# Optimization experiments

Hardware: AMD Instinct MI355X
Metric: run time of the kernel (lower is better)

The kernel has to match this reference:

```python
import jax, jax.numpy as jnp
import numpy as np

H = 3584          # hidden_size
NH = 28           # num query heads
NKV = 4           # num kv heads
HD = H // NH      # head_dim = 128
I = 18944         # intermediate_size
EPS = 1e-6
THETA = 1000000.0


def setup_inputs() -> dict:
    key = jax.random.key(0)
    ks = jax.random.split(key, 16)
    B, S = 1, 2048
    s = 0.02
    inp = {
        "hidden_states": jax.random.normal(ks[0], (B, S, H), jnp.float32),
        "position_ids": jnp.broadcast_to(jnp.arange(S, dtype=jnp.int32)[None, :], (B, S)),
        "q_w": jax.random.normal(ks[1], (NH * HD, H), jnp.float32) * s,
        "q_b": jax.random.normal(ks[2], (NH * HD,), jnp.float32) * s,
        "k_w": jax.random.normal(ks[3], (NKV * HD, H), jnp.float32) * s,
        "k_b": jax.random.normal(ks[4], (NKV * HD,), jnp.float32) * s,
        "v_w": jax.random.normal(ks[5], (NKV * HD, H), jnp.float32) * s,
        "v_b": jax.random.normal(ks[6], (NKV * HD,), jnp.float32) * s,
        "o_w": jax.random.normal(ks[7], (H, NH * HD), jnp.float32) * s,
        "gate_w": jax.random.normal(ks[8], (I, H), jnp.float32) * s,
        "up_w": jax.random.normal(ks[9], (I, H), jnp.float32) * s,
        "down_w": jax.random.normal(ks[10], (H, I), jnp.float32) * s,
        "ln1_w": jnp.ones((H,), jnp.float32),
        "ln2_w": jnp.ones((H,), jnp.float32),
    }
    return inp


def _rms_norm(x, w):
    var = jnp.mean(jnp.square(x), axis=-1, keepdims=True)
    return x * jax.lax.rsqrt(var + EPS) * w


def _rope_cos_sin(position_ids):
    # inv_freq: [HD/2]
    inv_freq = 1.0 / (THETA ** (jnp.arange(0, HD, 2, dtype=jnp.float32) / HD))
    ang = position_ids.astype(jnp.float32)[..., None] * inv_freq  # [B,S,HD/2]
    emb = jnp.concatenate([ang, ang], axis=-1)                     # [B,S,HD]
    return jnp.cos(emb)[:, None], jnp.sin(emb)[:, None]            # [B,1,S,HD]


def _rotate_half(x):
    x1, x2 = x[..., : HD // 2], x[..., HD // 2 :]
    return jnp.concatenate([-x2, x1], axis=-1)


def _forward(hidden_states, position_ids, q_w, q_b, k_w, k_b, v_w, v_b,
             o_w, gate_w, up_w, down_w, ln1_w, ln2_w):
    B, S, _ = hidden_states.shape
    residual = hidden_states
    x = _rms_norm(hidden_states, ln1_w)

    q = jnp.einsum("bsh,dh->bsd", x, q_w) + q_b   # [B,S,NH*HD]
    k = jnp.einsum("bsh,dh->bsd", x, k_w) + k_b   # [B,S,NKV*HD]
    v = jnp.einsum("bsh,dh->bsd", x, v_w) + v_b

    q = q.reshape(B, S, NH, HD).transpose(0, 2, 1, 3)    # [B,NH,S,HD]
    k = k.reshape(B, S, NKV, HD).transpose(0, 2, 1, 3)   # [B,NKV,S,HD]
    v = v.reshape(B, S, NKV, HD).transpose(0, 2, 1, 3)

    cos, sin = _rope_cos_sin(position_ids)
    q = q * cos + _rotate_half(q) * sin
    k = k * cos + _rotate_half(k) * sin

    # GQA: group query heads per kv head (NH = NKV * G)
    G = NH // NKV
    qg = q.reshape(B, NKV, G, S, HD)
    scores = jnp.einsum("bhgsd,bhtd->bhgst", qg, k) / jnp.sqrt(jnp.float32(HD))
    probs = jax.nn.softmax(scores, axis=-1)               # no causal mask in source
    attn = jnp.einsum("bhgst,bhtd->bhgsd", probs, v)      # [B,NKV,G,S,HD]
    attn = attn.reshape(B, NH, S, HD).transpose(0, 2, 1, 3).reshape(B, S, H)

    attn_out = jnp.einsum("bsd,hd->bsh", attn, o_w)
    hidden = residual + attn_out

    residual = hidden
    x = _rms_norm(hidden, ln2_w)
    gate = jax.nn.silu(jnp.einsum("bsh,ih->bsi", x, gate_w))
    up = jnp.einsum("bsh,ih->bsi", x, up_w)
    mlp = jnp.einsum("bsi,hi->bsh", gate * up, down_w)
    return residual + mlp


def reference(hidden_states, position_ids, q_w, q_b, k_w, k_b, v_w, v_b,
              o_w, gate_w, up_w, down_w, ln1_w, ln2_w):
    return _forward(hidden_states, position_ids, q_w, q_b, k_w, k_b, v_w, v_b,
                    o_w, gate_w, up_w, down_w, ln1_w, ln2_w)
```

## Files before the change

### kernel.cpp

```cpp
#include <hip/hip_runtime.h>
#include <hip/hip_bf16.h>
#include <stdint.h>

#define S_LEN 2048
#define HDIM  3584
#define NHEAD 28
#define NKVH  4
#define HDHD  128
#define IDIM  18944

typedef __attribute__((ext_vector_type(8))) short short8;
typedef __attribute__((ext_vector_type(4))) float floatx4;
typedef __attribute__((ext_vector_type(4))) unsigned int uint4v;

__device__ __forceinline__ unsigned short f2bf(float f) {
  union { float f; unsigned int u; } v; v.f = f;
  unsigned int r = v.u + 0x7fffu + ((v.u >> 16) & 1u);
  return (unsigned short)(r >> 16);
}
__device__ __forceinline__ float bf2f(unsigned short h) {
  union { unsigned int u; float f; } v; v.u = ((unsigned int)h) << 16;
  return v.f;
}
__device__ __forceinline__ unsigned int pk2(float a, float b) {
  __hip_bfloat162 h = __float22bfloat162_rn(make_float2(a, b));
  union { __hip_bfloat162 h; unsigned int u; } c; c.h = h; return c.u;
}

__device__ __forceinline__ void gload_lds16(const void* g, void* l) {
  __builtin_amdgcn_global_load_lds(
      (const __attribute__((address_space(1))) void*)g,
      (__attribute__((address_space(3))) void*)l, 16, 0, 0);
}

__device__ __forceinline__ int xcd_remap(int id, int total) {
  return (id & 7) * (total >> 3) + (id >> 3);
}

__device__ __forceinline__ void store_out(int MODE, void* outp, const void* aux,
                                          size_t oidx, float v) {
  if (MODE == 0) {
    ((float*)outp)[oidx] = v;
  } else if (MODE == 1) {
    ((unsigned short*)outp)[oidx] = f2bf(v);
  } else if (MODE == 2) {
    ((float*)outp)[oidx] = v + ((const float*)aux)[oidx];
  } else {
    float gt = bf2f(((const unsigned short*)aux)[oidx]);
    float sg = gt / (1.f + __expf(-gt));
    ((unsigned short*)outp)[oidx] = f2bf(sg * v);
  }
}

template<int MODE, bool BIAS>
__global__ __launch_bounds__(256)
void gemm_bf(const unsigned short* __restrict__ A, int lda,
             const unsigned short* __restrict__ W,
             const float* __restrict__ bias,
             void* __restrict__ outp, int ldo, int col0,
             const void* __restrict__ aux, int K)
{
  const int g  = xcd_remap(blockIdx.x, gridDim.x);
  const int mb = g & 15;
  const int nb = g >> 4;
  const int t = threadIdx.x;
  const int w = t >> 6, l = t & 63, lg = l >> 4, lc = l & 15;
  const int wr = w >> 1, wc = w & 1;

  __shared__ __align__(16) unsigned short As[128 * 64];
  __shared__ __align__(16) unsigned short Ws[128 * 64];

  floatx4 acc[4][4] = {};

  const char* Ablk = (const char*)(A + (size_t)mb * 128 * lda);
  const char* Wblk = (const char*)(W + (size_t)nb * 128 * K);

  const int s_row = t >> 3;
  const int s_scb = (((t & 7) ^ ((t >> 3) & 7)) << 4);
  const int r_sw  = (lc & 7) << 4;

  const size_t abytes = (size_t)lda * 2;
  const size_t wbytes = (size_t)K * 2;
  const int nk = K >> 6;
  for (int kt = 0; kt < nk; ++kt) {
    #pragma unroll
    for (int i = 0; i < 4; ++i)
      gload_lds16(Ablk + (size_t)(i * 32 + s_row) * abytes + (size_t)kt * 128 + s_scb,
                  (char*)As + i * 4096 + t * 16);
    #pragma unroll
    for (int i = 0; i < 4; ++i)
      gload_lds16(Wblk + (size_t)(i * 32 + s_row) * wbytes + (size_t)kt * 128 + s_scb,
                  (char*)Ws + i * 4096 + t * 16);
    __syncthreads();
    #pragma unroll
    for (int kk = 0; kk < 2; ++kk) {
      short8 afr[4], bfr[4];
      #pragma unroll
      for (int m = 0; m < 4; ++m)
        afr[m] = *(const short8*)((const char*)As + (wr*64 + m*16 + lc) * 128
                                 + ((kk*64 + lg*16) ^ r_sw));
      #pragma unroll
      for (int n = 0; n < 4; ++n)
        bfr[n] = *(const short8*)((const char*)Ws + (wc*64 + n*16 + lc) * 128
                                  + ((kk*64 + lg*16) ^ r_sw));
      #pragma unroll
      for (int m = 0; m < 4; ++m)
        #pragma unroll
        for (int n = 0; n < 4; ++n)
          acc[m][n] = __builtin_amdgcn_mfma_f32_16x16x32_bf16(afr[m], bfr[n], acc[m][n], 0, 0, 0);
    }
    __syncthreads();
  }

  float bv[4] = {0.f, 0.f, 0.f, 0.f};
  if (BIAS) {
    #pragma unroll
    for (int n = 0; n < 4; ++n) bv[n] = bias[nb*128 + wc*64 + n*16 + lc];
  }
  #pragma unroll
  for (int m = 0; m < 4; ++m) {
    #pragma unroll
    for (int n = 0; n < 4; ++n) {
      const int colg = col0 + nb*128 + wc*64 + n*16 + lc;
      #pragma unroll
      for (int j = 0; j < 4; ++j) {
        const int rowg = mb*128 + wr*64 + m*16 + lg*4 + j;
        store_out(MODE, outp, aux, (size_t)rowg * ldo + colg, acc[m][n][j] + bv[n]);
      }
    }
  }
}

template<int MODE, bool BIAS>
__global__ __launch_bounds__(256, 2)
void gemm_w(const unsigned short* __restrict__ A, int lda,
            const unsigned short* __restrict__ W,
            const float* __restrict__ bias,
            void* __restrict__ outp, int ldo, int col0,
            const void* __restrict__ aux, int K)
{
  const int g  = xcd_remap(blockIdx.x, gridDim.x);
  const int mb = g & 7;
  const int nb = g >> 3;
  const int t  = threadIdx.x;
  const int w  = t >> 6, l = t & 63, lg = l >> 4, lc = l & 15;
  const int wr = w >> 1, wc = w & 1;

  __shared__ __align__(16) unsigned short As[256 * 64];
  __shared__ __align__(16) unsigned short Bs[128 * 64];

  floatx4 acc[8][4] = {};

  const char* Ablk = (const char*)(A + (size_t)mb * 256 * lda);
  const char* Wblk = (const char*)(W + (size_t)nb * 128 * K);

  const int s_row = t >> 3;
  const int s_scb = (((t & 7) ^ ((t >> 3) & 7)) << 4);
  const int r_sw  = (lc & 7) << 4;

  const size_t abytes = (size_t)lda * 2;
  const size_t wbytes = (size_t)K * 2;
  const int nk = K >> 6;

  for (int kt = 0; kt < nk; ++kt) {
    const char* asrc = Ablk + (size_t)kt * 128 + s_scb;
    #pragma unroll
    for (int i = 0; i < 8; ++i)
      gload_lds16(asrc + (size_t)(i * 32 + s_row) * abytes,
                  (char*)As + i * 4096 + t * 16);
    const char* wsrc = Wblk + (size_t)kt * 128 + s_scb;
    #pragma unroll
    for (int i = 0; i < 4; ++i)
      gload_lds16(wsrc + (size_t)(i * 32 + s_row) * wbytes,
                  (char*)Bs + i * 4096 + t * 16);
    __syncthreads();
    #pragma unroll
    for (int kk = 0; kk < 2; ++kk) {
      const int ko = (kk * 64 + lg * 16) ^ r_sw;
      short8 bfr[4];
      #pragma unroll
      for (int n = 0; n < 4; ++n)
        bfr[n] = *(const short8*)((const char*)Bs + (wc*64 + n*16 + lc) * 128 + ko);
      #pragma unroll
      for (int m = 0; m < 8; ++m) {
        short8 af = *(const short8*)((const char*)As + (wr*128 + m*16 + lc) * 128 + ko);
        #pragma unroll
        for (int n = 0; n < 4; ++n)
          acc[m][n] = __builtin_amdgcn_mfma_f32_16x16x32_bf16(af, bfr[n], acc[m][n], 0, 0, 0);
      }
    }
    __syncthreads();
  }

  float bv[4] = {0.f, 0.f, 0.f, 0.f};
  if (BIAS) {
    #pragma unroll
    for (int n = 0; n < 4; ++n) bv[n] = bias[nb*128 + wc*64 + n*16 + lc];
  }
  #pragma unroll
  for (int m = 0; m < 8; ++m) {
    #pragma unroll
    for (int n = 0; n < 4; ++n) {
      const int colg = col0 + nb*128 + wc*64 + n*16 + lc;
      #pragma unroll
      for (int j = 0; j < 4; ++j) {
        const int rowg = mb*256 + wr*128 + m*16 + lg*4 + j;
        store_out(MODE, outp, aux, (size_t)rowg * ldo + colg, acc[m][n][j] + bv[n]);
      }
    }
  }
}

__global__ __launch_bounds__(256)
void cvt_bf16_kernel(const float* __restrict__ in, unsigned short* __restrict__ out, int n8)
{
  int i = blockIdx.x * 256 + threadIdx.x;
  const int stride = gridDim.x * 256;
  for (; i < n8; i += stride) {
    floatx4 a = *(const floatx4*)(in + (size_t)i * 8);
    floatx4 b = *(const floatx4*)(in + (size_t)i * 8 + 4);
    uint4v p;
    p[0] = pk2(a[0], a[1]); p[1] = pk2(a[2], a[3]);
    p[2] = pk2(b[0], b[1]); p[3] = pk2(b[2], b[3]);
    *(uint4v*)(out + (size_t)i * 8) = p;
  }
}

__global__ void pack_bias_kernel(const float* __restrict__ qb, const float* __restrict__ kb,
                                 const float* __restrict__ vb, float* __restrict__ o)
{
  int i = blockIdx.x * 256 + threadIdx.x;
  if (i < 3584) o[i] = qb[i];
  else if (i < 4096) o[i] = kb[i - 3584];
  else if (i < 4608) o[i] = vb[i - 4096];
}

__global__ __launch_bounds__(448)
void rmsnorm_kernel(const float* __restrict__ x, const float* __restrict__ wgt,
                    unsigned short* __restrict__ out)
{
  const int row = blockIdx.x, t = threadIdx.x;
  const float* xp = x + (size_t)row * HDIM + t * 8;
  floatx4 a = *(const floatx4*)xp;
  floatx4 b = *(const floatx4*)(xp + 4);
  float ss = a[0]*a[0]+a[1]*a[1]+a[2]*a[2]+a[3]*a[3]
           + b[0]*b[0]+b[1]*b[1]+b[2]*b[2]+b[3]*b[3];
  #pragma unroll
  for (int mk = 1; mk < 64; mk <<= 1) ss += __shfl_xor(ss, mk, 64);
  __shared__ float wsum[8];
  if ((t & 63) == 0) wsum[t >> 6] = ss;
  __syncthreads();
  float tot = 0.f;
  #pragma unroll
  for (int i = 0; i < 7; ++i) tot += wsum[i];
  const float sc = rsqrtf(tot * (1.f / 3584.f) + 1e-6f);
  const float* wp = wgt + t * 8;
  short8 o;
  #pragma unroll
  for (int e = 0; e < 4; ++e) o[e]   = (short)f2bf(a[e] * sc * wp[e]);
  #pragma unroll
  for (int e = 0; e < 4; ++e) o[4+e] = (short)f2bf(b[e] * sc * wp[4+e]);
  *(short8*)(out + (size_t)row * HDIM + t * 8) = o;
}

__global__ void rope_table_kernel(const int* __restrict__ pos, float* __restrict__ tab)
{
  int idx = blockIdx.x * 256 + threadIdx.x;
  int s = idx >> 6, d = idx & 63;
  float p = (float)pos[s];
  float inv = expf(-((float)(2 * d) * (1.f / 128.f)) * 13.815510557964274f);
  float ang = p * inv;
  tab[idx] = cosf(ang);
  tab[S_LEN * 64 + idx] = sinf(ang);
}

template<int NHX>
__global__ void rope_apply_kernel(const float* __restrict__ in, const float* __restrict__ tab,
                                  unsigned short* __restrict__ out, int col0)
{
  int idx = blockIdx.x * 256 + threadIdx.x;
  int d = idx & 63;
  int rem = idx >> 6;
  int hh = rem % NHX;
  int s  = rem / NHX;
  const float* ip = in + (size_t)s * 4608 + col0 + hh * HDHD;
  float x1 = ip[d], x2 = ip[64 + d];
  float c  = tab[s * 64 + d];
  float sn = tab[S_LEN * 64 + s * 64 + d];
  unsigned short* op = out + (size_t)s * (NHX * HDHD) + hh * HDHD;
  op[d]      = f2bf(x1 * c - x2 * sn);
  op[64 + d] = f2bf(x2 * c + x1 * sn);
}

__global__ void vtrans_kernel(const float* __restrict__ qkvf, unsigned short* __restrict__ vt)
{
  int idx = blockIdx.x * 256 + threadIdx.x;
  int s = idx & (S_LEN - 1);
  int c = idx >> 11;
  vt[idx] = f2bf(qkvf[(size_t)s * 4608 + 4096 + c]);
}

__global__ __launch_bounds__(512)
void attn_kernel(const unsigned short* __restrict__ Q,
                 const unsigned short* __restrict__ Kr,
                 const unsigned short* __restrict__ Vt,
                 unsigned short* __restrict__ O)
{
  const int g  = xcd_remap(blockIdx.x, gridDim.x);
  const int qb = g & 15;
  const int h  = g >> 4;
  const int kvh = h / 7;
  const int t = threadIdx.x, w = t >> 6, l = t & 63, lg = l >> 4, lc = l & 15;

  __shared__ __align__(16) unsigned short Ks[64 * 128];
  __shared__ __align__(16) unsigned short Vs[128 * 64];
  __shared__ __align__(16) unsigned short Ps[8][16 * 64];

  const int qrow = qb * 128 + w * 16 + lc;
  short8 qf[4];
  {
    const unsigned short* qp = Q + (size_t)qrow * HDIM + h * HDHD + lg * 8;
    #pragma unroll
    for (int kk = 0; kk < 4; ++kk) qf[kk] = *(const short8*)(qp + kk * 32);
  }

  float mrun[4], lrun[4];
  #pragma unroll
  for (int j = 0; j < 4; ++j) { mrun[j] = -1e30f; lrun[j] = 0.f; }
  floatx4 oacc[8] = {};

  const int k_row = t >> 4;
  const int k_scb = (((t & 15) ^ ((t >> 4) & 7)) << 4);
  const int v_row = t >> 3;
  const int v_scb = (((t & 7) ^ ((t >> 3) & 7)) << 4);
  const int r_sw  = (lc & 7) << 4;
  const float scale = 0.08838834764831843f;

  for (int kt = 0; kt < 32; ++kt) {
    #pragma unroll
    for (int i = 0; i < 2; ++i)
      gload_lds16((const char*)Kr + ((size_t)(kt*64 + i*32 + k_row) * 512 + kvh*128) * 2 + k_scb,
                  (char*)Ks + i * 8192 + t * 16);
    #pragma unroll
    for (int i = 0; i < 2; ++i)
      gload_lds16((const char*)Vt + ((size_t)(kvh*128 + i*64 + v_row) * S_LEN) * 2
                      + (size_t)kt * 128 + v_scb,
                  (char*)Vs + i * 8192 + t * 16);
    __syncthreads();

    floatx4 sacc[4] = {};
    #pragma unroll
    for (int kk = 0; kk < 4; ++kk) {
      #pragma unroll
      for (int n = 0; n < 4; ++n) {
        short8 kf = *(const short8*)((const char*)Ks + (n*16 + lc) * 256
                                     + ((kk*64 + lg*16) ^ r_sw));
        sacc[n] = __builtin_amdgcn_mfma_f32_16x16x32_bf16(qf[kk], kf, sacc[n], 0, 0, 0);
      }
    }

    float pv[4][4], mt[4];
    #pragma unroll
    for (int j = 0; j < 4; ++j) {
      float a0 = sacc[0][j]*scale, a1 = sacc[1][j]*scale;
      float a2 = sacc[2][j]*scale, a3 = sacc[3][j]*scale;
      pv[0][j]=a0; pv[1][j]=a1; pv[2][j]=a2; pv[3][j]=a3;
      mt[j] = fmaxf(fmaxf(a0, a1), fmaxf(a2, a3));
    }
    #pragma unroll
    for (int mk = 1; mk < 16; mk <<= 1)
      #pragma unroll
      for (int j = 0; j < 4; ++j)
        mt[j] = fmaxf(mt[j], __shfl_xor(mt[j], mk, 16));

    float corr[4], rs[4];
    #pragma unroll
    for (int j = 0; j < 4; ++j) {
      float mn = fmaxf(mrun[j], mt[j]);
      corr[j] = __expf(mrun[j] - mn);
      mrun[j] = mn;
      rs[j] = 0.f;
    }
    #pragma unroll
    for (int n = 0; n < 4; ++n)
      #pragma unroll
      for (int j = 0; j < 4; ++j) {
        float p = __expf(pv[n][j] - mrun[j]);
        pv[n][j] = p; rs[j] += p;
      }
    #pragma unroll
    for (int mk = 1; mk < 16; mk <<= 1)
      #pragma unroll
      for (int j = 0; j < 4; ++j)
        rs[j] += __shfl_xor(rs[j], mk, 16);
    #pragma unroll
    for (int j = 0; j < 4; ++j) lrun[j] = lrun[j] * corr[j] + rs[j];
    #pragma unroll
    for (int q = 0; q < 8; ++q) {
      oacc[q][0] *= corr[0]; oacc[q][1] *= corr[1];
      oacc[q][2] *= corr[2]; oacc[q][3] *= corr[3];
    }

    char* pw = (char*)Ps[w];
    #pragma unroll
    for (int n = 0; n < 4; ++n)
      #pragma unroll
      for (int j = 0; j < 4; ++j) {
        const int prow = lg*4 + j;
        *(unsigned short*)(pw + prow*128 + ((((n*16 + lc)*2)) ^ ((prow & 7) << 4)))
            = f2bf(pv[n][j]);
      }

    short8 pa[2];
    #pragma unroll
    for (int ks = 0; ks < 2; ++ks)
      pa[ks] = *(const short8*)(pw + lc*128 + ((ks*64 + lg*16) ^ r_sw));
    #pragma unroll
    for (int ks = 0; ks < 2; ++ks)
      #pragma unroll
      for (int q = 0; q < 8; ++q) {
        short8 vf = *(const short8*)((const char*)Vs + (q*16 + lc) * 128
                                     + ((ks*64 + lg*16) ^ r_sw));
        oacc[q] = __builtin_amdgcn_mfma_f32_16x16x32_bf16(pa[ks], vf, oacc[q], 0, 0, 0);
      }
    __syncthreads();
  }

  float invl[4];
  #pragma unroll
  for (int j = 0; j < 4; ++j) invl[j] = 1.f / lrun[j];
  #pragma unroll
  for (int q = 0; q < 8; ++q)
    #pragma unroll
    for (int j = 0; j < 4; ++j) {
      int rowg = qb*128 + w*16 + lg*4 + j;
      int colg = h*HDHD + q*16 + lc;
      O[(size_t)rowg * HDIM + colg] = f2bf(oacc[q][j] * invl[j]);
    }
}

__global__ void sentinel_kernel(float* out, int n) {
  int i = blockIdx.x * 256 + threadIdx.x;
  if (i < n) out[i] = 1.0e6f;
}

extern "C" void kernel_launch(void* const* d_in, const int* in_sizes, int n_in,
                              void* d_out, int out_size, void* d_ws, size_t ws_size,
                              hipStream_t stream)
{
  (void)in_sizes; (void)n_in;
  const float* hidden = (const float*)d_in[0];
  const int*   pos    = (const int*)d_in[1];
  const float* q_w    = (const float*)d_in[2];
  const float* q_b    = (const float*)d_in[3];
  const float* k_w    = (const float*)d_in[4];
  const float* k_b    = (const float*)d_in[5];
  const float* v_w    = (const float*)d_in[6];
  const float* v_b    = (const float*)d_in[7];
  const float* o_w    = (const float*)d_in[8];
  const float* gate_w = (const float*)d_in[9];
  const float* up_w   = (const float*)d_in[10];
  const float* down_w = (const float*)d_in[11];
  const float* ln1    = (const float*)d_in[12];
  const float* ln2    = (const float*)d_in[13];
  float* out = (float*)d_out;
  char* ws = (char*)d_ws;

  unsigned short* XN    = (unsigned short*)(ws + 0);
  float*          QKVF  = (float*)(ws + 14680064);
  unsigned short* QR    = (unsigned short*)(ws + 52428800);
  unsigned short* KR    = (unsigned short*)(ws + 67108864);
  unsigned short* VT    = (unsigned short*)(ws + 69206016);
  float*          ROPET = (float*)(ws + 71303168);
  float*          BQKV  = (float*)(ws + 72351744);
  unsigned short* CTX   = (unsigned short*)(ws + 77594624);
  unsigned short* GBUF  = (unsigned short*)(ws + 0);
  unsigned short* ACT   = (unsigned short*)(ws + 77594624);
  float*          H1    = (float*)(ws + 155189248);
  unsigned short* XN2   = (unsigned short*)(ws + 184549376);
  unsigned short* WB    = (unsigned short*)(ws + 199229440);
  const size_t NEED_BIG = 199229440 + 135790592;

  if (ws_size < NEED_BIG) {
    sentinel_kernel<<<(out_size + 255) / 256, 256, 0, stream>>>(out, out_size);
    return;
  }

  const int CVG = 2048;

  rope_table_kernel<<<(S_LEN * 64) / 256, 256, 0, stream>>>(pos, ROPET);
  rmsnorm_kernel<<<S_LEN, 448, 0, stream>>>(hidden, ln1, XN);

  pack_bias_kernel<<<18, 256, 0, stream>>>(q_b, k_b, v_b, BQKV);
  cvt_bf16_kernel<<<CVG, 256, 0, stream>>>(q_w, WB,               (3584 * 3584) / 8);
  cvt_bf16_kernel<<<CVG, 256, 0, stream>>>(k_w, WB + 3584 * 3584, (512 * 3584) / 8);
  cvt_bf16_kernel<<<CVG, 256, 0, stream>>>(v_w, WB + 4096 * 3584, (512 * 3584) / 8);

  gemm_w<0, true><<<288, 256, 0, stream>>>(XN, HDIM, WB, BQKV, QKVF, 4608, 0, nullptr, HDIM);

  rope_apply_kernel<28><<<(S_LEN * 28 * 64) / 256, 256, 0, stream>>>(QKVF, ROPET, QR, 0);
  rope_apply_kernel<4><<<(S_LEN * 4 * 64) / 256,  256, 0, stream>>>(QKVF, ROPET, KR, 3584);
  vtrans_kernel<<<(512 * S_LEN) / 256, 256, 0, stream>>>(QKVF, VT);

  cvt_bf16_kernel<<<CVG, 256, 0, stream>>>(o_w, WB, (3584 * 3584) / 8);

  attn_kernel<<<448, 512, 0, stream>>>(QR, KR, VT, CTX);

  gemm_w<2, false><<<224, 256, 0, stream>>>(CTX, HDIM, WB, nullptr, H1, HDIM, 0, hidden, HDIM);
  rmsnorm_kernel<<<S_LEN, 448, 0, stream>>>(H1, ln2, XN2);

  cvt_bf16_kernel<<<CVG, 256, 0, stream>>>(gate_w, WB, (IDIM * HDIM) / 8);
  gemm_w<1, false><<<1184, 256, 0, stream>>>(XN2, HDIM, WB, nullptr, GBUF, IDIM, 0, nullptr, HDIM);

  cvt_bf16_kernel<<<CVG, 256, 0, stream>>>(up_w, WB, (IDIM * HDIM) / 8);
  gemm_w<3, false><<<1184, 256, 0, stream>>>(XN2, HDIM, WB, nullptr, ACT, IDIM, 0, GBUF, HDIM);

  cvt_bf16_kernel<<<CVG, 256, 0, stream>>>(down_w, WB, (HDIM * IDIM) / 8);
  gemm_bf<2, false><<<448, 256, 0, stream>>>(ACT, IDIM, WB, nullptr, out, HDIM, 0, H1, IDIM);
}
```

Baseline: 1.651 ms.

## Add 256x256-tile 8-wave ping-pong GEMM for gate and up projections

Adds a new bf16 MFMA GEMM kernel that uses 512-thread blocks with 256x256 output tiles and double-buffered LDS A/B stages, split into eight phases that interleave global-to-LDS loads with MFMA bursts. It uses explicit barriers, setprio and waitcnt control. The gate and up projections switch from the previous 256-thread kernel with 1184 blocks to this kernel with 592 blocks. The goal is better data reuse per tile and overlap of memory traffic with matrix math in the two largest GEMMs. The cost is a large LDS footprint (128 KB) and more complex synchronisation.

```diff
diff --git a/kernel.cpp b/kernel.cpp
--- a/kernel.cpp
+++ b/kernel.cpp
@@ -209,6 +209,167 @@
       }
     }
   }
+}
+
+#define RD_A(par, mu)                                                          \
+  do {                                                                         \
+    const char* _b = (const char*)Ab[par][wr];                                 \
+    _Pragma("unroll")                                                          \
+    for (int m = 0; m < 4; ++m)                                                \
+      _Pragma("unroll")                                                        \
+      for (int kk = 0; kk < 2; ++kk)                                           \
+        af[m][kk] = *(const short8*)(_b + ((mu)*64 + m*16 + lc) * 128          \
+                                     + ((kk*64 + lg*16) ^ r_sw));              \
+  } while (0)
+
+#define RD_B(par, nu, bf)                                                      \
+  do {                                                                         \
+    const char* _b = (const char*)Bb[par][bh];                                 \
+    _Pragma("unroll")                                                          \
+    for (int n = 0; n < 2; ++n)                                                \
+      _Pragma("unroll")                                                        \
+      for (int kk = 0; kk < 2; ++kk)                                           \
+        bf[n][kk] = *(const short8*)(_b + (brl + (nu)*32 + n*16 + lc) * 128    \
+                                     + ((kk*64 + lg*16) ^ r_sw));              \
+  } while (0)
+
+#define MFMA16(mu, nu, bf)                                                     \
+  do {                                                                         \
+    __builtin_amdgcn_s_setprio(1);                                             \
+    _Pragma("unroll")                                                          \
+    for (int m = 0; m < 4; ++m)                                                \
+      _Pragma("unroll")                                                        \
+      for (int n = 0; n < 2; ++n)                                              \
+        _Pragma("unroll")                                                      \
+        for (int kk = 0; kk < 2; ++kk)                                         \
+          acc[mu][nu][m][n] = __builtin_amdgcn_mfma_f32_16x16x32_bf16(         \
+              af[m][kk], bf[n][kk], acc[mu][nu][m][n], 0, 0, 0);               \
+    __builtin_amdgcn_s_setprio(0);                                             \
+  } while (0)
+
+#define PH_BAR()                                                               \
+  do {                                                                         \
+    __builtin_amdgcn_sched_barrier(0);                                         \
+    __builtin_amdgcn_s_barrier();                                              \
+    asm volatile("s_waitcnt lgkmcnt(0)" ::: "memory");                         \
+    __builtin_amdgcn_sched_barrier(0);                                         \
+  } while (0)
+
+#define PH_END()                                                               \
+  do {                                                                         \
+    __builtin_amdgcn_sched_barrier(0);                                         \
+    __builtin_amdgcn_s_barrier();                                              \
+    __builtin_amdgcn_sched_barrier(0);                                         \
+  } while (0)
+
+template<int MODE>
+__global__ __launch_bounds__(512)
+void gemm_8p2(const unsigned short* __restrict__ A, int lda,
+              const unsigned short* __restrict__ W,
+              void* __restrict__ outp, int ldo,
+              const void* __restrict__ aux, int K)
+{
+  const int g  = xcd_remap(blockIdx.x, gridDim.x);
+  const int mb = g & 7;
+  const int nb = g >> 3;
+  const int t  = threadIdx.x;
+  const int w  = t >> 6, l = t & 63, lg = l >> 4, lc = l & 15;
+  const int wr  = w >> 2;
+  const int wc  = w & 3;
+  const int bh  = wc >> 1;
+  const int brl = (wc & 1) * 64;
+
+  __shared__ __align__(16) unsigned short Ab[2][2][128 * 64];
+  __shared__ __align__(16) unsigned short Bb[2][2][128 * 64];
+
+  floatx4 acc[2][2][4][2] = {};
+
+  const char* Ablk = (const char*)(A + (size_t)mb * 256 * lda);
+  const char* Wblk = (const char*)(W + (size_t)nb * 256 * K);
+
+  const int srow = t >> 3;
+  const int scb  = (((t & 7) ^ ((t >> 3) & 7)) << 4);
+  const int r_sw = (lc & 7) << 4;
+
+  const size_t ab = (size_t)lda * 2;
+  const size_t wb2 = (size_t)K * 2;
+
+  auto stage_a = [&](int par, int half, int kt) {
+    const char* src = Ablk + (size_t)(half * 128) * ab + (size_t)kt * 128 + scb;
+    char* dst = (char*)Ab[par][half] + t * 16;
+    gload_lds16(src + (size_t)srow * ab, dst);
+    gload_lds16(src + (size_t)(64 + srow) * ab, dst + 8192);
+  };
+  auto stage_b = [&](int par, int half, int kt) {
+    const char* src = Wblk + (size_t)(half * 128) * wb2 + (size_t)kt * 128 + scb;
+    char* dst = (char*)Bb[par][half] + t * 16;
+    gload_lds16(src + (size_t)srow * wb2, dst);
+    gload_lds16(src + (size_t)(64 + srow) * wb2, dst + 8192);
+  };
+
+  const int NT = K >> 6;
+  stage_b(0, 0, 0); stage_b(0, 1, 0); stage_a(0, 0, 0); stage_a(0, 1, 0);
+  stage_b(1, 0, 1); stage_b(1, 1, 1);
+  asm volatile("s_waitcnt vmcnt(0)" ::: "memory");
+  __builtin_amdgcn_sched_barrier(0);
+  __builtin_amdgcn_s_barrier();
+  __builtin_amdgcn_sched_barrier(0);
+
+  short8 af[4][2], b0[2][2], b1[2][2];
+
+  for (int j = 0; j < (NT >> 1); ++j) {
+    const int t1 = 2 * j + 1;
+    const int t2 = (2 * j + 2 < NT) ? (2 * j + 2) : 0;
+    const int t3 = (2 * j + 3 < NT) ? (2 * j + 3) : 1;
+
+    RD_A(0, 0); RD_B(0, 0, b0);
+    stage_a(1, 0, t1);
+    PH_BAR(); MFMA16(0, 0, b0); PH_END();
+
+    RD_B(0, 1, b1);
+    stage_a(1, 1, t1);
+    PH_BAR(); MFMA16(0, 1, b1); PH_END();
+
+    RD_A(0, 1);
+    stage_b(0, 0, t2);
+    PH_BAR(); MFMA16(1, 1, b1); PH_END();
+
+    stage_b(0, 1, t2);
+    asm volatile("s_waitcnt vmcnt(4)" ::: "memory");
+    PH_BAR(); MFMA16(1, 0, b0); PH_END();
+
+    RD_A(1, 0); RD_B(1, 0, b0);
+    stage_a(0, 0, t2);
+    PH_BAR(); MFMA16(0, 0, b0); PH_END();
+
+    RD_B(1, 1, b1);
+    stage_a(0, 1, t2);
+    PH_BAR(); MFMA16(0, 1, b1); PH_END();
+
+    RD_A(1, 1);
+    stage_b(1, 0, t3);
+    PH_BAR(); MFMA16(1, 1, b1); PH_END();
+
+    stage_b(1, 1, t3);
+    asm volatile("s_waitcnt vmcnt(4)" ::: "memory");
+    PH_BAR(); MFMA16(1, 0, b0); PH_END();
+  }
+
+  #pragma unroll
+  for (int mu = 0; mu < 2; ++mu)
+    #pragma unroll
+    for (int nu = 0; nu < 2; ++nu)
+      #pragma unroll
+      for (int m = 0; m < 4; ++m)
+        #pragma unroll
+        for (int n = 0; n < 2; ++n) {
+          const int colg = nb*256 + bh*128 + brl + nu*32 + n*16 + lc;
+          #pragma unroll
+          for (int jj = 0; jj < 4; ++jj) {
+            const int rowg = mb*256 + wr*128 + mu*64 + m*16 + lg*4 + jj;
+            store_out(MODE, outp, aux, (size_t)rowg * ldo + colg, acc[mu][nu][m][n][jj]);
+          }
+        }
 }
 
 __global__ __launch_bounds__(256)
@@ -510,10 +671,10 @@
   rmsnorm_kernel<<<S_LEN, 448, 0, stream>>>(H1, ln2, XN2);
 
   cvt_bf16_kernel<<<CVG, 256, 0, stream>>>(gate_w, WB, (IDIM * HDIM) / 8);
-  gemm_w<1, false><<<1184, 256, 0, stream>>>(XN2, HDIM, WB, nullptr, GBUF, IDIM, 0, nullptr, HDIM);
+  gemm_8p2<1><<<592, 512, 0, stream>>>(XN2, HDIM, WB, GBUF, IDIM, nullptr, HDIM);
 
   cvt_bf16_kernel<<<CVG, 256, 0, stream>>>(up_w, WB, (IDIM * HDIM) / 8);
-  gemm_w<3, false><<<1184, 256, 0, stream>>>(XN2, HDIM, WB, nullptr, ACT, IDIM, 0, GBUF, HDIM);
+  gemm_8p2<3><<<592, 512, 0, stream>>>(XN2, HDIM, WB, ACT, IDIM, GBUF, HDIM);
 
   cvt_bf16_kernel<<<CVG, 256, 0, stream>>>(down_w, WB, (HDIM * IDIM) / 8);
   gemm_bf<2, false><<<448, 256, 0, stream>>>(ACT, IDIM, WB, nullptr, out, HDIM, 0, H1, IDIM);
```

After: 1.857 ms. 12.5% more time.
